# Kernel optimization log

Hardware: AMD Instinct MI355X
Metric: run time of the kernel (lower is better)

The kernel has to match this reference:

```python
import jax, jax.numpy as jnp
import numpy as np


def _w2_1d(u, v):
    """Squared W2 distance between two 1D densities on grid positions arange(n)/n."""
    u = u / (jnp.sum(u) + 1e-10)
    v = v / (jnp.sum(v) + 1e-10)
    u_cdf = jnp.cumsum(u)                       # [n]
    v_cdf = jnp.cumsum(v)                       # [n]
    qs = jnp.sort(jnp.concatenate([u_cdf, v_cdf]))  # [2n]
    n = u.shape[0]
    pos = jnp.arange(n, dtype=u.dtype) / n      # support positions (n == m here)
    # quantile functions via searchsorted (side='left', same as torch default) + clamped gather
    u_q = pos[jnp.clip(jnp.searchsorted(u_cdf, qs), 0, n - 1)]
    v_q = pos[jnp.clip(jnp.searchsorted(v_cdf, qs), 0, n - 1)]
    delta = jnp.diff(qs, prepend=0.0)           # qs padded with leading zero, then diff
    return jnp.sum(delta * (u_q - v_q) ** 2)    # p = 2


def setup_inputs() -> dict:
    key = jax.random.key(0)
    k1, k2 = jax.random.split(key)
    B, S, T, R = 4, 8, 2048, 256
    x = jax.random.normal(k1, (B, S, T, R), dtype=jnp.float32)
    y = jax.random.normal(k2, (B, S, T, R), dtype=jnp.float32)
    return {"x": x, "y": y}


def reference(x, y):
    B, S, T, R = x.shape
    # transform_nonnegative, method='linear': shift by 1.1 * global min (if negative)
    mn = jnp.minimum(jnp.min(x), jnp.min(y))
    mn = jnp.where(mn < 0, mn, jnp.zeros((), x.dtype))
    x = x - 1.1 * mn
    y = y - 1.1 * mn
    # normalize along time axis (dim=2), sum-to-1
    x = x / jnp.sum(x, axis=2, keepdims=True)
    y = y / jnp.sum(y, axis=2, keepdims=True)
    # flatten (B, S, R) problems; each 1D distribution lives along the time axis
    xr = jnp.transpose(x, (0, 1, 3, 2)).reshape(-1, T)  # [B*S*R, T]
    yr = jnp.transpose(y, (0, 1, 3, 2)).reshape(-1, T)
    w2 = jax.vmap(_w2_1d)(xr, yr).reshape(B, S, R)
    return jnp.sum(w2, axis=(1, 2))  # loss per batch element, shape [B]
```

## Files before the change

### kernel.cpp

```cpp
#include <hip/hip_runtime.h>

#define T_N 2048
#define R_N 256
#define SLICES 32
#define NELEM (SLICES * T_N * R_N)
#define INFV 3.0e38f
#define MIN_BLOCKS 2048
#define MIN_THREADS (MIN_BLOCKS * 256)

__global__ __launch_bounds__(256) void kmin(const float* __restrict__ x,
                                            const float* __restrict__ y,
                                            float* __restrict__ partial,
                                            float* __restrict__ out) {
    if (blockIdx.x == 0 && threadIdx.x < 4) out[threadIdx.x] = 0.0f;
    const int g0 = blockIdx.x * 256 + threadIdx.x;
    const float4* __restrict__ x4 = (const float4*)x;
    const float4* __restrict__ y4 = (const float4*)y;
    float m0 = INFV, m1 = INFV;
    #pragma unroll
    for (int half = 0; half < 2; ++half) {
        float4 va[4], vb[4];
        #pragma unroll
        for (int it = 0; it < 4; ++it) {
            const int idx = g0 + (half * 4 + it) * MIN_THREADS;
            va[it] = x4[idx];
            vb[it] = y4[idx];
        }
        #pragma unroll
        for (int it = 0; it < 4; ++it) {
            m0 = fminf(m0, fminf(fminf(va[it].x, va[it].y), fminf(va[it].z, va[it].w)));
            m1 = fminf(m1, fminf(fminf(vb[it].x, vb[it].y), fminf(vb[it].z, vb[it].w)));
        }
    }
    float m = fminf(m0, m1);
    #pragma unroll
    for (int off = 32; off; off >>= 1) m = fminf(m, __shfl_down(m, off));
    __shared__ float sm[4];
    if ((threadIdx.x & 63) == 0) sm[threadIdx.x >> 6] = m;
    __syncthreads();
    if (threadIdx.x == 0)
        partial[blockIdx.x] = fminf(fminf(sm[0], sm[1]), fminf(sm[2], sm[3]));
}

__global__ __launch_bounds__(1024, 8) void kmain(const float* __restrict__ x,
                                                 const float* __restrict__ y,
                                                 const float* __restrict__ partial,
                                                 float* __restrict__ out) {
    __shared__ float L[8 * T_N];
    __shared__ float red16[16];
    __shared__ float psum[4][2][4];
    __shared__ float pacc[4][4];

    const int tid = threadIdx.x;
    const int w = tid >> 6;
    const int lane = tid & 63;

    {
        float m = fminf(partial[tid], partial[tid + 1024]);
        #pragma unroll
        for (int off = 32; off; off >>= 1) m = fminf(m, __shfl_down(m, off));
        if (lane == 0) red16[w] = m;
    }
    __syncthreads();
    float mn = red16[0];
    #pragma unroll
    for (int k = 1; k < 16; ++k) mn = fminf(mn, red16[k]);
    const float sh = 1.1f * fminf(mn, 0.0f);

    const int blk = blockIdx.x;
    const int xcd = blk & 7;
    const int k2 = blk >> 3;
    const int sub = k2 & 3;
    const int rest = k2 >> 2;
    const int rt = (((rest & 1) << 3) + xcd) * 4 + sub;
    const int bs = rest >> 1;
    const size_t base = (size_t)bs * (T_N * R_N) + (size_t)(rt * 4);

    #pragma unroll
    for (int it = 0; it < 2; ++it) {
        const int t = tid + 1024 * it;
        const float4 a = *(const float4*)(x + base + (size_t)t * R_N);
        const float4 b = *(const float4*)(y + base + (size_t)t * R_N);
        L[0 * T_N + t] = a.x - sh;  L[2 * T_N + t] = a.y - sh;
        L[4 * T_N + t] = a.z - sh;  L[6 * T_N + t] = a.w - sh;
        L[1 * T_N + t] = b.x - sh;  L[3 * T_N + t] = b.y - sh;
        L[5 * T_N + t] = b.z - sh;  L[7 * T_N + t] = b.w - sh;
    }
    __syncthreads();

    const int p  = w >> 2;
    const int wl = w & 3;
    const int pl = (wl << 6) | lane;
    float* __restrict__ cu = &L[(2 * p) * T_N];
    float* __restrict__ cv = &L[(2 * p + 1) * T_N];

    {
        float4* __restrict__ cu4 = (float4*)cu;
        float4* __restrict__ cv4 = (float4*)cv;
        float4 u0 = cu4[2 * pl], u1 = cu4[2 * pl + 1];
        float4 v0 = cv4[2 * pl], v1 = cv4[2 * pl + 1];
        const float su = ((u0.x + u0.y) + (u0.z + u0.w)) + ((u1.x + u1.y) + (u1.z + u1.w));
        const float sv = ((v0.x + v0.y) + (v0.z + v0.w)) + ((v1.x + v1.y) + (v1.z + v1.w));
        float iu = su, iv = sv;
        #pragma unroll
        for (int off = 1; off < 64; off <<= 1) {
            const float a = __shfl_up(iu, off);
            const float b = __shfl_up(iv, off);
            if (lane >= off) { iu += a; iv += b; }
        }
        if (lane == 63) { psum[p][0][wl] = iu; psum[p][1][wl] = iv; }
        __syncthreads();
        float prefU = 0.f, totU = 0.f, prefV = 0.f, totV = 0.f;
        #pragma unroll
        for (int k = 0; k < 4; ++k) {
            const float a = psum[p][0][k], b = psum[p][1][k];
            totU += a; totV += b;
            if (k < wl) { prefU += a; prefV += b; }
        }
        const float invU = 1.0f / totU, invV = 1.0f / totV;
        float ru = prefU + (iu - su);
        float rv = prefV + (iv - sv);
        float4 o;
        ru += u0.x; o.x = ru * invU; ru += u0.y; o.y = ru * invU;
        ru += u0.z; o.z = ru * invU; ru += u0.w; o.w = ru * invU;
        cu4[2 * pl] = o;
        ru += u1.x; o.x = ru * invU; ru += u1.y; o.y = ru * invU;
        ru += u1.z; o.z = ru * invU; ru += u1.w; o.w = ru * invU;
        cu4[2 * pl + 1] = o;
        rv += v0.x; o.x = rv * invV; rv += v0.y; o.y = rv * invV;
        rv += v0.z; o.z = rv * invV; rv += v0.w; o.w = rv * invV;
        cv4[2 * pl] = o;
        rv += v1.x; o.x = rv * invV; rv += v1.y; o.y = rv * invV;
        rv += v1.z; o.z = rv * invV; rv += v1.w; o.w = rv * invV;
        cv4[2 * pl + 1] = o;
    }
    __syncthreads();

    const int d = pl << 4;
    int i = 0, j = 0;
    if (d > 0) {
        int lo = (d > T_N) ? (d - T_N) : 0;
        int hi = (d < T_N) ? d : T_N;
        while (lo < hi) {
            const int mid = (lo + hi) >> 1;
            if (cu[mid] <= cv[d - mid - 1]) lo = mid + 1; else hi = mid;
        }
        i = lo; j = d - lo;
    }
    float qprev = 0.0f;
    if (d > 0) {
        const float pa_ = (i > 0) ? cu[i - 1] : -INFV;
        const float pb_ = (j > 0) ? cv[j - 1] : -INFV;
        qprev = fmaxf(pa_, pb_);
    }

    float uv = (i < T_N) ? cu[min(i, T_N - 1)] : INFV;
    float vv = (j < T_N) ? cv[min(j, T_N - 1)] : INFV;

    float acc = 0.0f;
    #pragma unroll
    for (int s = 0; s < 16; ++s) {
        const bool take = (uv <= vv);
        const float q = take ? uv : vv;
        const float dd = (float)(min(i, T_N - 1) - min(j, T_N - 1));
        acc += (q - qprev) * dd * dd;
        qprev = q;
        i += take ? 1 : 0;
        j += take ? 0 : 1;
        if (s < 15) {
            const int ni = take ? i : j;
            const float* bp = take ? cu : cv;
            const float r = bp[min(ni, T_N - 1)];
            const float rr = (ni < T_N) ? r : INFV;
            uv = take ? rr : uv;
            vv = take ? vv : rr;
        }
    }

    #pragma unroll
    for (int off = 32; off; off >>= 1) acc += __shfl_down(acc, off);
    if (lane == 0) pacc[p][wl] = acc;
    __syncthreads();
    if (tid == 0) {
        float r = 0.f;
        #pragma unroll
        for (int pp = 0; pp < 4; ++pp)
            r += (pacc[pp][0] + pacc[pp][1]) + (pacc[pp][2] + pacc[pp][3]);
        atomicAdd(&out[bs >> 3], r * (1.0f / ((float)T_N * (float)T_N)));
    }
}

extern "C" void kernel_launch(void* const* d_in, const int* in_sizes, int n_in,
                              void* d_out, int out_size, void* d_ws, size_t ws_size,
                              hipStream_t stream) {
    const float* x = (const float*)d_in[0];
    const float* y = (const float*)d_in[1];
    float* out = (float*)d_out;
    float* partial = (float*)d_ws;

    kmin<<<MIN_BLOCKS, 256, 0, stream>>>(x, y, partial, out);
    kmain<<<SLICES * 64, 1024, 0, stream>>>(x, y, partial, out);
}
```

Before: 209.5 us.

## Split merge-path into two interleaved 8-step chains with padded LDS sentinels

Each thread now handles two independent merge-path segments of 8 steps instead of one of 16. It runs the two binary searches interleaved with a fixed 11-iteration branchless loop. Rows in shared memory are padded with INF sentinels, which removes the bounds clamps, and the next candidates are prefetched one step ahead so the merge loop is not a serial LDS-latency chain. The cost is more registers and an extra binary search per thread.

```diff
diff --git a/kernel.cpp b/kernel.cpp
--- a/kernel.cpp
+++ b/kernel.cpp
@@ -7,6 +7,7 @@
 #define INFV 3.0e38f
 #define MIN_BLOCKS 2048
 #define MIN_THREADS (MIN_BLOCKS * 256)
+#define LSTR 2056
 
 __global__ __launch_bounds__(256) void kmin(const float* __restrict__ x,
                                             const float* __restrict__ y,
@@ -46,7 +47,7 @@
                                                  const float* __restrict__ y,
                                                  const float* __restrict__ partial,
                                                  float* __restrict__ out) {
-    __shared__ float L[8 * T_N];
+    __shared__ float L[8 * LSTR];
     __shared__ float red16[16];
     __shared__ float psum[4][2][4];
     __shared__ float pacc[4][4];
@@ -76,23 +77,25 @@
     const int bs = rest >> 1;
     const size_t base = (size_t)bs * (T_N * R_N) + (size_t)(rt * 4);
 
+    if (tid < 64) L[(tid >> 3) * LSTR + T_N + (tid & 7)] = INFV;
+
     #pragma unroll
     for (int it = 0; it < 2; ++it) {
         const int t = tid + 1024 * it;
         const float4 a = *(const float4*)(x + base + (size_t)t * R_N);
         const float4 b = *(const float4*)(y + base + (size_t)t * R_N);
-        L[0 * T_N + t] = a.x - sh;  L[2 * T_N + t] = a.y - sh;
-        L[4 * T_N + t] = a.z - sh;  L[6 * T_N + t] = a.w - sh;
-        L[1 * T_N + t] = b.x - sh;  L[3 * T_N + t] = b.y - sh;
-        L[5 * T_N + t] = b.z - sh;  L[7 * T_N + t] = b.w - sh;
+        L[0 * LSTR + t] = a.x - sh;  L[2 * LSTR + t] = a.y - sh;
+        L[4 * LSTR + t] = a.z - sh;  L[6 * LSTR + t] = a.w - sh;
+        L[1 * LSTR + t] = b.x - sh;  L[3 * LSTR + t] = b.y - sh;
+        L[5 * LSTR + t] = b.z - sh;  L[7 * LSTR + t] = b.w - sh;
     }
     __syncthreads();
 
     const int p  = w >> 2;
     const int wl = w & 3;
     const int pl = (wl << 6) | lane;
-    float* __restrict__ cu = &L[(2 * p) * T_N];
-    float* __restrict__ cv = &L[(2 * p + 1) * T_N];
+    float* __restrict__ cu = &L[(2 * p) * LSTR];
+    float* __restrict__ cv = &L[(2 * p + 1) * LSTR];
 
     {
         float4* __restrict__ cu4 = (float4*)cu;
@@ -136,46 +139,72 @@
     }
     __syncthreads();
 
-    const int d = pl << 4;
-    int i = 0, j = 0;
-    if (d > 0) {
-        int lo = (d > T_N) ? (d - T_N) : 0;
-        int hi = (d < T_N) ? d : T_N;
-        while (lo < hi) {
-            const int mid = (lo + hi) >> 1;
-            if (cu[mid] <= cv[d - mid - 1]) lo = mid + 1; else hi = mid;
-        }
-        i = lo; j = d - lo;
-    }
-    float qprev = 0.0f;
-    if (d > 0) {
-        const float pa_ = (i > 0) ? cu[i - 1] : -INFV;
-        const float pb_ = (j > 0) ? cv[j - 1] : -INFV;
-        qprev = fmaxf(pa_, pb_);
-    }
-
-    float uv = (i < T_N) ? cu[min(i, T_N - 1)] : INFV;
-    float vv = (j < T_N) ? cv[min(j, T_N - 1)] : INFV;
-
-    float acc = 0.0f;
-    #pragma unroll
-    for (int s = 0; s < 16; ++s) {
-        const bool take = (uv <= vv);
-        const float q = take ? uv : vv;
-        const float dd = (float)(min(i, T_N - 1) - min(j, T_N - 1));
-        acc += (q - qprev) * dd * dd;
-        qprev = q;
-        i += take ? 1 : 0;
-        j += take ? 0 : 1;
-        if (s < 15) {
-            const int ni = take ? i : j;
-            const float* bp = take ? cu : cv;
-            const float r = bp[min(ni, T_N - 1)];
-            const float rr = (ni < T_N) ? r : INFV;
-            uv = take ? rr : uv;
-            vv = take ? vv : rr;
-        }
-    }
+    const int dA = pl << 4;
+    const int dB = dA + 8;
+    int loA = max(0, dA - T_N), hiA = min(dA, T_N);
+    int loB = max(0, dB - T_N), hiB = min(dB, T_N);
+    for (int it = 0; it < 11; ++it) {
+        const int mA = (loA + hiA) >> 1;
+        const int mB = (loB + hiB) >> 1;
+        const float aA = cu[mA];
+        const float bA = cv[max(dA - mA - 1, 0)];
+        const float aB = cu[mB];
+        const float bB = cv[max(dB - mB - 1, 0)];
+        const bool gA = loA < hiA, gB = loB < hiB;
+        const bool cA = gA && (aA <= bA);
+        const bool cB = gB && (aB <= bB);
+        loA = cA ? mA + 1 : loA;
+        hiA = (gA && !cA) ? mA : hiA;
+        loB = cB ? mB + 1 : loB;
+        hiB = (gB && !cB) ? mB : hiB;
+    }
+    int iA = loA, jA = dA - loA;
+    int iB = loB, jB = dB - loB;
+
+    float qpA = 0.0f;
+    if (dA > 0) {
+        const float pa_ = (iA > 0) ? cu[iA - 1] : -INFV;
+        const float pb_ = (jA > 0) ? cv[jA - 1] : -INFV;
+        qpA = fmaxf(pa_, pb_);
+    }
+    float qpB;
+    {
+        const float pa_ = (iB > 0) ? cu[iB - 1] : -INFV;
+        const float pb_ = (jB > 0) ? cv[jB - 1] : -INFV;
+        qpB = fmaxf(pa_, pb_);
+    }
+
+    float uvA = cu[iA], vvA = cv[jA], puA = cu[iA + 1], pvA = cv[jA + 1];
+    float uvB = cu[iB], vvB = cv[jB], puB = cu[iB + 1], pvB = cv[jB + 1];
+    float accA = 0.0f, accB = 0.0f;
+    #pragma unroll
+    for (int s = 0; s < 8; ++s) {
+        {
+            const bool take = (uvA <= vvA);
+            const float q = fminf(uvA, vvA);
+            const float dd = (float)(min(iA, T_N - 1) - min(jA, T_N - 1));
+            accA += (q - qpA) * dd * dd;
+            qpA = q;
+            iA += take ? 1 : 0;
+            jA += take ? 0 : 1;
+            uvA = take ? puA : uvA;
+            vvA = take ? vvA : pvA;
+            if (s < 7) { puA = cu[iA + 1]; pvA = cv[jA + 1]; }
+        }
+        {
+            const bool take = (uvB <= vvB);
+            const float q = fminf(uvB, vvB);
+            const float dd = (float)(min(iB, T_N - 1) - min(jB, T_N - 1));
+            accB += (q - qpB) * dd * dd;
+            qpB = q;
+            iB += take ? 1 : 0;
+            jB += take ? 0 : 1;
+            uvB = take ? puB : uvB;
+            vvB = take ? vvB : pvB;
+            if (s < 7) { puB = cu[iB + 1]; pvB = cv[jB + 1]; }
+        }
+    }
+    float acc = accA + accB;
 
     #pragma unroll
     for (int off = 32; off; off >>= 1) acc += __shfl_down(acc, off);
```

Result: slower. 222.0 us (+6.0%).
